# Kernel optimization log

Measured on AMD Instinct MI355X. Metric: run time of the kernel, lower is better.

Reference implementation:

```python
import jax, jax.numpy as jnp
import numpy as np

N_NODES = 100000
N_EDGES = 1000000
IN_CH, HID_CH, N_CLS = 128, 64, 40


def setup_inputs() -> dict:
    key = jax.random.key(0)
    ks = jax.random.split(key, 8)
    x = jax.random.normal(ks[0], (N_NODES, IN_CH), dtype=jnp.float32)
    edge_index = jax.random.randint(ks[1], (2, N_EDGES), 0, N_NODES, dtype=jnp.int32)
    # Glorot-ish scaled weights (ARMAConv init_weight / root_weight, K=1 stack squeezed)
    w1_init = jax.random.normal(ks[2], (IN_CH, HID_CH), dtype=jnp.float32) / np.sqrt(IN_CH)
    w1_root = jax.random.normal(ks[3], (IN_CH, HID_CH), dtype=jnp.float32) / np.sqrt(IN_CH)
    b1 = jnp.zeros((HID_CH,), dtype=jnp.float32)
    w2_init = jax.random.normal(ks[4], (HID_CH, N_CLS), dtype=jnp.float32) / np.sqrt(HID_CH)
    w2_root = jax.random.normal(ks[5], (HID_CH, N_CLS), dtype=jnp.float32) / np.sqrt(HID_CH)
    b2 = jnp.zeros((N_CLS,), dtype=jnp.float32)
    return {"x": x, "edge_index": edge_index,
            "w1_init": w1_init, "w1_root": w1_root, "b1": b1,
            "w2_init": w2_init, "w2_root": w2_root, "b2": b2}


def _arma_layer(x, row, col, norm, w_init, w_root, bias):
    # ARMAConv, num_stacks=1, num_layers=1, shared_weights=True, eval mode (dropout=id):
    # out = relu( A_hat @ (x W_init) + x W_root + b ), mean over the single stack.
    h = x @ w_init                           # [N, F_out]
    msg = norm[:, None] * h[row]             # gather from source nodes, [E, F_out]
    agg = jax.ops.segment_sum(msg, col, num_segments=N_NODES)  # scatter-add at targets
    return jax.nn.relu(agg + x @ w_root + bias)


def reference(x, edge_index, w1_init, w1_root, b1, w2_init, w2_root, b2):
    row, col = edge_index[0], edge_index[1]
    # gcn_norm, add_self_loops=False: deg over targets, norm = d^-1/2[row] * d^-1/2[col]
    deg = jax.ops.segment_sum(jnp.ones((row.shape[0],), x.dtype), col, num_segments=N_NODES)
    dinv = jnp.where(deg > 0, jax.lax.rsqrt(jnp.maximum(deg, 1e-12)), jnp.zeros_like(deg))
    norm = dinv[row] * dinv[col]
    h = _arma_layer(x, row, col, norm, w1_init, w1_root, b1)
    h = jax.nn.relu(h)  # BiARMA relu; dropout identity in eval
    return _arma_layer(h, row, col, norm, w2_init, w2_root, b2)
```

## Files before the change

kernel.cpp:

```cpp
#include <hip/hip_runtime.h>

#define N_NODES 100000
#define N_EDGES 1000000
#define IN_CH 128
#define HID_CH 64
#define N_CLS 40

#define NBUCK 782

static inline int cdiv(int a, int b) { return (a + b - 1) / b; }

__device__ __forceinline__ unsigned pack_bf2(float a, float b) {
    unsigned ua = __float_as_uint(a), ub = __float_as_uint(b);
    ua += 0x7fffu + ((ua >> 16) & 1u);
    ub += 0x7fffu + ((ub >> 16) & 1u);
    return (ua >> 16) | (ub & 0xffff0000u);
}
__device__ __forceinline__ float bf_lo(unsigned u) { return __uint_as_float(u << 16); }
__device__ __forceinline__ float bf_hi(unsigned u) { return __uint_as_float(u & 0xffff0000u); }


__global__ __launch_bounds__(256)
void bucket_count_kernel(const int* __restrict__ cols, int* __restrict__ gcount, int E) {
    __shared__ int hist[NBUCK];
    for (int i = threadIdx.x; i < NBUCK; i += 256) hist[i] = 0;
    __syncthreads();
    int per = (E + gridDim.x - 1) / gridDim.x;
    int s = blockIdx.x * per;
    int e = min(E, s + per);
    for (int j = s + threadIdx.x; j < e; j += 256)
        atomicAdd(&hist[cols[j] >> 7], 1);
    __syncthreads();
    for (int i = threadIdx.x; i < NBUCK; i += 256)
        if (hist[i]) atomicAdd(&gcount[i], hist[i]);
}


__global__ __launch_bounds__(1024)
void scan_bucket_kernel(const int* __restrict__ gcount, int* __restrict__ boff,
                        int* __restrict__ gcursor, int* __restrict__ offsets) {
    __shared__ int part[1024];
    int t = threadIdx.x;
    part[t] = (t < NBUCK) ? gcount[t] : 0;
    __syncthreads();
    for (int off = 1; off < 1024; off <<= 1) {
        int v = (t >= off) ? part[t - off] : 0;
        __syncthreads();
        part[t] += v;
        __syncthreads();
    }
    int excl = (t > 0) ? part[t - 1] : 0;
    if (t < NBUCK) { boff[t] = excl; gcursor[t] = excl; }
    if (t == NBUCK) { boff[NBUCK] = excl; offsets[N_NODES] = excl; }
}


__global__ __launch_bounds__(256)
void bucket_scatter_kernel(const int* __restrict__ rows, const int* __restrict__ cols,
                           int* __restrict__ gcursor, int* __restrict__ pedge, int E) {
    __shared__ int cur[NBUCK];
    for (int i = threadIdx.x; i < NBUCK; i += 256) cur[i] = 0;
    __syncthreads();
    int per = (E + gridDim.x - 1) / gridDim.x;
    int s = blockIdx.x * per;
    int e = min(E, s + per);
    for (int j = s + threadIdx.x; j < e; j += 256)
        atomicAdd(&cur[cols[j] >> 7], 1);
    __syncthreads();
    for (int i = threadIdx.x; i < NBUCK; i += 256) {
        int h = cur[i];
        cur[i] = h ? atomicAdd(&gcursor[i], h) : 0;
    }
    __syncthreads();
    for (int j = s + threadIdx.x; j < e; j += 256) {
        int c = cols[j];
        int pos = atomicAdd(&cur[c >> 7], 1);
        pedge[pos] = (rows[j] << 7) | (c & 127);
    }
}


__global__ __launch_bounds__(256)
void bucket_sort_kernel(const int* __restrict__ boff, const int* __restrict__ pedge,
                        int* __restrict__ srow, int* __restrict__ offsets,
                        float* __restrict__ dinv) {
    __shared__ int cnt[128];
    __shared__ int scn[128];
    __shared__ int cur[128];
    int b = blockIdx.x, t = threadIdx.x;
    if (t < 128) cnt[t] = 0;
    __syncthreads();
    int e0 = boff[b], e1 = boff[b + 1];
    for (int j = e0 + t; j < e1; j += 256)
        atomicAdd(&cnt[pedge[j] & 127], 1);
    __syncthreads();
    if (t < 128) scn[t] = cnt[t];
    __syncthreads();
    for (int off = 1; off < 128; off <<= 1) {
        int v = 0;
        if (t < 128 && t >= off) v = scn[t - off];
        __syncthreads();
        if (t < 128) scn[t] += v;
        __syncthreads();
    }
    if (t < 128) {
        int excl = (t > 0) ? scn[t - 1] : 0;
        cur[t] = excl;
        int node = b * 128 + t;
        if (node < N_NODES) {
            offsets[node] = e0 + excl;
            dinv[node] = cnt[t] ? rsqrtf((float)cnt[t]) : 0.f;
        }
    }
    __syncthreads();
    for (int j = e0 + t; j < e1; j += 256) {
        int p = pedge[j];
        int pos = atomicAdd(&cur[p & 127], 1);
        srow[e0 + pos] = p >> 7;
    }
}


template<int K, int C1, int C2>
__launch_bounds__(256, 4)
__global__ void gemm_fused_kernel(const float* __restrict__ X,
                                  const float* __restrict__ W1,
                                  const float* __restrict__ W2,
                                  const float* __restrict__ Bias,
                                  const float* __restrict__ dinv,
                                  unsigned* __restrict__ Y1b,
                                  float* __restrict__ Y2, int N) {
    constexpr int CT = C1 + C2;
    constexpr int CB = (CT - 64) / 16;
    constexpr int RPT = 4;
    constexpr int KC = 32;
    constexpr int NCHUNK = K / KC;
    static_assert(CT == 128 || CT == 80, "layout");
    static_assert(C1 % 4 == 0 && C2 % 4 == 0, "vec4");

    __shared__ float wl[KC][CT];
    __shared__ float xs[64][KC + 4];

    const int tid = threadIdx.x;
    const int r0 = blockIdx.x * 64;
    const int tcol = tid & 15;
    const int trow = tid >> 4;
    const int ca = tcol * 4;
    const int cb = 64 + tcol * CB;
    const int rbase = trow * RPT;

    float bsA[4];
#pragma unroll
    for (int j = 0; j < 4; ++j)
        bsA[j] = (ca >= C1) ? Bias[ca - C1 + j] : 0.f;
    float bsB[CB];
#pragma unroll
    for (int j = 0; j < CB; ++j)
        bsB[j] = Bias[cb - C1 + j];

    float accA[RPT][4];
    float accB[RPT][CB];
#pragma unroll
    for (int i = 0; i < RPT; ++i) {
#pragma unroll
        for (int j = 0; j < 4; ++j) accA[i][j] = 0.f;
#pragma unroll
        for (int j = 0; j < CB; ++j) accB[i][j] = 0.f;
    }

    for (int ch = 0; ch < NCHUNK; ++ch) {
        __syncthreads();
        constexpr int W1F4 = KC * C1 / 4;
        constexpr int W2F4 = KC * C2 / 4;
        for (int i = tid; i < W1F4; i += 256) {
            int kk = i / (C1 / 4);
            int f4 = i - kk * (C1 / 4);
            float4 v = *reinterpret_cast<const float4*>(&W1[(size_t)(ch * KC + kk) * C1 + f4 * 4]);
            *reinterpret_cast<float4*>(&wl[kk][f4 * 4]) = v;
        }
        for (int i = tid; i < W2F4; i += 256) {
            int kk = i / (C2 / 4);
            int f4 = i - kk * (C2 / 4);
            float4 v = *reinterpret_cast<const float4*>(&W2[(size_t)(ch * KC + kk) * C2 + f4 * 4]);
            *reinterpret_cast<float4*>(&wl[kk][C1 + f4 * 4]) = v;
        }
        constexpr int XF4 = 64 * KC / 4;
        for (int i = tid; i < XF4; i += 256) {
            int rr = i / (KC / 4);
            int k4 = i - rr * (KC / 4);
            int gr = r0 + rr;
            float4 v = make_float4(0.f, 0.f, 0.f, 0.f);
            if (gr < N)
                v = *reinterpret_cast<const float4*>(&X[(size_t)gr * K + ch * KC + k4 * 4]);
            *reinterpret_cast<float4*>(&xs[rr][k4 * 4]) = v;
        }
        __syncthreads();
#pragma unroll 8
        for (int kk = 0; kk < KC; ++kk) {
            float xv[RPT];
#pragma unroll
            for (int i = 0; i < RPT; ++i) xv[i] = xs[rbase + i][kk];
            float4 wA = *reinterpret_cast<const float4*>(&wl[kk][ca]);
            float wB[CB];
            if constexpr (CB == 4) {
                float4 w4 = *reinterpret_cast<const float4*>(&wl[kk][cb]);
                wB[0] = w4.x; wB[1] = w4.y; wB[2] = w4.z; wB[3] = w4.w;
            } else {
                wB[0] = wl[kk][cb];
            }
#pragma unroll
            for (int i = 0; i < RPT; ++i) {
                accA[i][0] = fmaf(xv[i], wA.x, accA[i][0]);
                accA[i][1] = fmaf(xv[i], wA.y, accA[i][1]);
                accA[i][2] = fmaf(xv[i], wA.z, accA[i][2]);
                accA[i][3] = fmaf(xv[i], wA.w, accA[i][3]);
#pragma unroll
                for (int j = 0; j < CB; ++j)
                    accB[i][j] = fmaf(xv[i], wB[j], accB[i][j]);
            }
        }
    }

#pragma unroll
    for (int i = 0; i < RPT; ++i) {
        int r = r0 + rbase + i;
        if (r >= N) continue;
        if (ca < C1) {
            float dr = dinv[r];
            uint2 p;
            p.x = pack_bf2(accA[i][0] * dr, accA[i][1] * dr);
            p.y = pack_bf2(accA[i][2] * dr, accA[i][3] * dr);
            *reinterpret_cast<uint2*>(&Y1b[((size_t)r * C1 + ca) >> 1]) = p;
        } else {
            float4 v = make_float4(accA[i][0] + bsA[0], accA[i][1] + bsA[1],
                                   accA[i][2] + bsA[2], accA[i][3] + bsA[3]);
            *reinterpret_cast<float4*>(&Y2[(size_t)r * C2 + (ca - C1)]) = v;
        }
        if constexpr (CB == 4) {
            float4 v = make_float4(accB[i][0] + bsB[0], accB[i][1] + bsB[1],
                                   accB[i][2] + bsB[2], accB[i][3] + bsB[3]);
            *reinterpret_cast<float4*>(&Y2[(size_t)r * C2 + (cb - C1)]) = v;
        } else {
            Y2[(size_t)r * C2 + (cb - C1)] = accB[i][0] + bsB[0];
        }
    }
}


template<int C>
__launch_bounds__(256)
__global__ void pull_bf16_kernel(const int* __restrict__ offsets,
                                 const int* __restrict__ srow,
                                 const float* __restrict__ dinv,
                                 const unsigned* __restrict__ H,
                                 float* __restrict__ Y, int N) {
    constexpr int TPE = C / 4;
    constexpr int CH = C / 2;
    int gid = blockIdx.x * blockDim.x + threadIdx.x;
    int node = gid / TPE;
    int lane = gid - node * TPE;
    if (node >= N) return;

    int e0 = offsets[node];
    int e1 = offsets[node + 1];
    float dc = dinv[node];

    float4 acc = make_float4(0.f, 0.f, 0.f, 0.f);
    int j = e0;
    for (; j + 4 <= e1; j += 4) {
        int r0 = srow[j + 0];
        int r1 = srow[j + 1];
        int r2 = srow[j + 2];
        int r3 = srow[j + 3];
        uint2 u0 = *reinterpret_cast<const uint2*>(&H[(size_t)r0 * CH + lane * 2]);
        uint2 u1 = *reinterpret_cast<const uint2*>(&H[(size_t)r1 * CH + lane * 2]);
        uint2 u2 = *reinterpret_cast<const uint2*>(&H[(size_t)r2 * CH + lane * 2]);
        uint2 u3 = *reinterpret_cast<const uint2*>(&H[(size_t)r3 * CH + lane * 2]);
        acc.x += (bf_lo(u0.x) + bf_lo(u1.x)) + (bf_lo(u2.x) + bf_lo(u3.x));
        acc.y += (bf_hi(u0.x) + bf_hi(u1.x)) + (bf_hi(u2.x) + bf_hi(u3.x));
        acc.z += (bf_lo(u0.y) + bf_lo(u1.y)) + (bf_lo(u2.y) + bf_lo(u3.y));
        acc.w += (bf_hi(u0.y) + bf_hi(u1.y)) + (bf_hi(u2.y) + bf_hi(u3.y));
    }
    for (; j < e1; ++j) {
        int r = srow[j];
        uint2 u = *reinterpret_cast<const uint2*>(&H[(size_t)r * CH + lane * 2]);
        acc.x += bf_lo(u.x);
        acc.y += bf_hi(u.x);
        acc.z += bf_lo(u.y);
        acc.w += bf_hi(u.y);
    }

    float4* Y4 = reinterpret_cast<float4*>(Y);
    size_t yi = (size_t)node * TPE + lane;
    float4 y = Y4[yi];
    y.x = fmaxf(fmaf(dc, acc.x, y.x), 0.f);
    y.y = fmaxf(fmaf(dc, acc.y, y.y), 0.f);
    y.z = fmaxf(fmaf(dc, acc.z, y.z), 0.f);
    y.w = fmaxf(fmaf(dc, acc.w, y.w), 0.f);
    Y4[yi] = y;
}


extern "C" void kernel_launch(void* const* d_in, const int* in_sizes, int n_in,
                              void* d_out, int out_size, void* d_ws, size_t ws_size,
                              hipStream_t stream) {
    const float* x       = (const float*)d_in[0];
    const int*   eidx    = (const int*)d_in[1];
    const float* w1_init = (const float*)d_in[2];
    const float* w1_root = (const float*)d_in[3];
    const float* b1      = (const float*)d_in[4];
    const float* w2_init = (const float*)d_in[5];
    const float* w2_root = (const float*)d_in[6];
    const float* b2      = (const float*)d_in[7];
    float* out = (float*)d_out;

    const int* rows = eidx;
    const int* cols = eidx + N_EDGES;

    int* wsi = (int*)d_ws;
    int*      gcount  = wsi;
    int*      boff    = wsi + 784;
    int*      gcursor = wsi + 1572;
    float*    dinv    = (float*)(wsi + 2360);
    int*      offsets = wsi + 102360;
    int*      srow    = wsi + 202364;
    unsigned* h0b     = (unsigned*)(wsi + 1202364);
    int*      pedge   = wsi + 1202364;
    float*    agg1    = (float*)(wsi + 4402364);
    unsigned* h2b     = h0b;

    hipMemsetAsync(gcount, 0, 784 * sizeof(int), stream);
    bucket_count_kernel<<<128, 256, 0, stream>>>(cols, gcount, N_EDGES);
    scan_bucket_kernel<<<1, 1024, 0, stream>>>(gcount, boff, gcursor, offsets);
    bucket_scatter_kernel<<<128, 256, 0, stream>>>(rows, cols, gcursor, pedge, N_EDGES);
    bucket_sort_kernel<<<NBUCK, 256, 0, stream>>>(boff, pedge, srow, offsets, dinv);

    const int GGRID = cdiv(N_NODES, 64);

    gemm_fused_kernel<IN_CH, HID_CH, HID_CH><<<GGRID, 256, 0, stream>>>(
        x, w1_init, w1_root, b1, dinv, h0b, agg1, N_NODES);
    pull_bf16_kernel<HID_CH><<<cdiv(N_NODES * (HID_CH / 4), 256), 256, 0, stream>>>(
        offsets, srow, dinv, h0b, agg1, N_NODES);

    gemm_fused_kernel<HID_CH, N_CLS, N_CLS><<<GGRID, 256, 0, stream>>>(
        agg1, w2_init, w2_root, b2, dinv, h2b, out, N_NODES);
    pull_bf16_kernel<N_CLS><<<cdiv(N_NODES * (N_CLS / 4), 256), 256, 0, stream>>>(
        offsets, srow, dinv, h2b, out, N_NODES);
}
```

Before: 287.5 us.

## Replace FP32 FMA dense GEMM with bf16 MFMA matrix-core kernel

The fused dual-weight GEMM now converts X and W tiles to bf16 in shared memory and computes with 16x16x32 bf16 MFMA instructions instead of scalar FP32 FMAs, with each wave handling 16 rows. The whole K dimension is staged at once, with weights transposed into a padded layout. This targets the compute cost of the two dense projections. In exchange it lowers the precision of the root/bias path (now bf16 inputs) and writes scalar, less coalesced outputs per lane.

```diff
diff --git a/kernel.cpp b/kernel.cpp
--- a/kernel.cpp
+++ b/kernel.cpp
@@ -10,11 +10,19 @@
 
 static inline int cdiv(int a, int b) { return (a + b - 1) / b; }
 
+using bf16x8 = __attribute__((ext_vector_type(8))) short;
+using f32x4  = __attribute__((ext_vector_type(4))) float;
+
 __device__ __forceinline__ unsigned pack_bf2(float a, float b) {
     unsigned ua = __float_as_uint(a), ub = __float_as_uint(b);
     ua += 0x7fffu + ((ua >> 16) & 1u);
     ub += 0x7fffu + ((ub >> 16) & 1u);
     return (ua >> 16) | (ub & 0xffff0000u);
+}
+__device__ __forceinline__ unsigned short bf16_of(float a) {
+    unsigned ua = __float_as_uint(a);
+    ua += 0x7fffu + ((ua >> 16) & 1u);
+    return (unsigned short)(ua >> 16);
 }
 __device__ __forceinline__ float bf_lo(unsigned u) { return __uint_as_float(u << 16); }
 __device__ __forceinline__ float bf_hi(unsigned u) { return __uint_as_float(u & 0xffff0000u); }
@@ -122,126 +130,102 @@
 
 
 template<int K, int C1, int C2>
-__launch_bounds__(256, 4)
-__global__ void gemm_fused_kernel(const float* __restrict__ X,
-                                  const float* __restrict__ W1,
-                                  const float* __restrict__ W2,
-                                  const float* __restrict__ Bias,
-                                  const float* __restrict__ dinv,
-                                  unsigned* __restrict__ Y1b,
-                                  float* __restrict__ Y2, int N) {
+__launch_bounds__(256)
+__global__ void gemm_mfma_fused_kernel(const float* __restrict__ X,
+                                       const float* __restrict__ W1,
+                                       const float* __restrict__ W2,
+                                       const float* __restrict__ Bias,
+                                       const float* __restrict__ dinv,
+                                       unsigned short* __restrict__ Y1b,
+                                       float* __restrict__ Y2, int N) {
     constexpr int CT = C1 + C2;
-    constexpr int CB = (CT - 64) / 16;
-    constexpr int RPT = 4;
-    constexpr int KC = 32;
-    constexpr int NCHUNK = K / KC;
-    static_assert(CT == 128 || CT == 80, "layout");
-    static_assert(C1 % 4 == 0 && C2 % 4 == 0, "vec4");
-
-    __shared__ float wl[KC][CT];
-    __shared__ float xs[64][KC + 4];
+    constexpr int NT = CT / 16;
+    constexpr int KS = K / 32;
+    constexpr int KP = (K + 8) / 2;
+    static_assert(CT % 16 == 0 && K % 32 == 0, "shape");
+    static_assert(C1 % 4 == 0 && C2 % 4 == 0, "staging vec4");
+
+    __shared__ unsigned xb[64 * KP];
+    __shared__ unsigned wt[CT * KP];
+    __shared__ float dloc[64];
 
     const int tid = threadIdx.x;
+    const int wave = tid >> 6;
+    const int lane = tid & 63;
+    const int m = lane & 15;
+    const int quad = lane >> 4;
     const int r0 = blockIdx.x * 64;
-    const int tcol = tid & 15;
-    const int trow = tid >> 4;
-    const int ca = tcol * 4;
-    const int cb = 64 + tcol * CB;
-    const int rbase = trow * RPT;
-
-    float bsA[4];
-#pragma unroll
-    for (int j = 0; j < 4; ++j)
-        bsA[j] = (ca >= C1) ? Bias[ca - C1 + j] : 0.f;
-    float bsB[CB];
-#pragma unroll
-    for (int j = 0; j < CB; ++j)
-        bsB[j] = Bias[cb - C1 + j];
-
-    float accA[RPT][4];
-    float accB[RPT][CB];
-#pragma unroll
-    for (int i = 0; i < RPT; ++i) {
-#pragma unroll
-        for (int j = 0; j < 4; ++j) accA[i][j] = 0.f;
-#pragma unroll
-        for (int j = 0; j < CB; ++j) accB[i][j] = 0.f;
-    }
-
-    for (int ch = 0; ch < NCHUNK; ++ch) {
-        __syncthreads();
-        constexpr int W1F4 = KC * C1 / 4;
-        constexpr int W2F4 = KC * C2 / 4;
-        for (int i = tid; i < W1F4; i += 256) {
-            int kk = i / (C1 / 4);
-            int f4 = i - kk * (C1 / 4);
-            float4 v = *reinterpret_cast<const float4*>(&W1[(size_t)(ch * KC + kk) * C1 + f4 * 4]);
-            *reinterpret_cast<float4*>(&wl[kk][f4 * 4]) = v;
+
+    if (tid < 64) {
+        int gr = r0 + tid;
+        dloc[tid] = (gr < N) ? dinv[gr] : 0.f;
+    }
+
+    constexpr int XIT = 64 * (K / 4);
+    for (int i = tid; i < XIT; i += 256) {
+        int rr = i / (K / 4);
+        int k4 = i - rr * (K / 4);
+        int gr = r0 + rr;
+        float4 v = make_float4(0.f, 0.f, 0.f, 0.f);
+        if (gr < N)
+            v = *reinterpret_cast<const float4*>(&X[(size_t)gr * K + k4 * 4]);
+        uint2 p;
+        p.x = pack_bf2(v.x, v.y);
+        p.y = pack_bf2(v.z, v.w);
+        *reinterpret_cast<uint2*>(&xb[rr * KP + k4 * 2]) = p;
+    }
+
+    constexpr int WIT = (K / 2) * (CT / 4);
+    for (int i = tid; i < WIT; i += 256) {
+        int kp = i / (CT / 4);
+        int c4 = i - kp * (CT / 4);
+        int k = kp * 2;
+        int c = c4 * 4;
+        float4 va, vb;
+        if (c < C1) {
+            va = *reinterpret_cast<const float4*>(&W1[(size_t)k * C1 + c]);
+            vb = *reinterpret_cast<const float4*>(&W1[(size_t)(k + 1) * C1 + c]);
+        } else {
+            va = *reinterpret_cast<const float4*>(&W2[(size_t)k * C2 + (c - C1)]);
+            vb = *reinterpret_cast<const float4*>(&W2[(size_t)(k + 1) * C2 + (c - C1)]);
         }
-        for (int i = tid; i < W2F4; i += 256) {
-            int kk = i / (C2 / 4);
-            int f4 = i - kk * (C2 / 4);
-            float4 v = *reinterpret_cast<const float4*>(&W2[(size_t)(ch * KC + kk) * C2 + f4 * 4]);
-            *reinterpret_cast<float4*>(&wl[kk][C1 + f4 * 4]) = v;
+        wt[(c + 0) * KP + kp] = pack_bf2(va.x, vb.x);
+        wt[(c + 1) * KP + kp] = pack_bf2(va.y, vb.y);
+        wt[(c + 2) * KP + kp] = pack_bf2(va.z, vb.z);
+        wt[(c + 3) * KP + kp] = pack_bf2(va.w, vb.w);
+    }
+    __syncthreads();
+
+    const int rowbase = wave * 16;
+    f32x4 acc[NT];
+#pragma unroll
+    for (int t = 0; t < NT; ++t) acc[t] = (f32x4){0.f, 0.f, 0.f, 0.f};
+
+#pragma unroll
+    for (int ks = 0; ks < KS; ++ks) {
+        bf16x8 a = *reinterpret_cast<const bf16x8*>(&xb[(rowbase + m) * KP + ks * 16 + quad * 4]);
+#pragma unroll
+        for (int t = 0; t < NT; ++t) {
+            bf16x8 b = *reinterpret_cast<const bf16x8*>(&wt[(t * 16 + m) * KP + ks * 16 + quad * 4]);
+            acc[t] = __builtin_amdgcn_mfma_f32_16x16x32_bf16(a, b, acc[t], 0, 0, 0);
         }
-        constexpr int XF4 = 64 * KC / 4;
-        for (int i = tid; i < XF4; i += 256) {
-            int rr = i / (KC / 4);
-            int k4 = i - rr * (KC / 4);
-            int gr = r0 + rr;
-            float4 v = make_float4(0.f, 0.f, 0.f, 0.f);
-            if (gr < N)
-                v = *reinterpret_cast<const float4*>(&X[(size_t)gr * K + ch * KC + k4 * 4]);
-            *reinterpret_cast<float4*>(&xs[rr][k4 * 4]) = v;
-        }
-        __syncthreads();
-#pragma unroll 8
-        for (int kk = 0; kk < KC; ++kk) {
-            float xv[RPT];
-#pragma unroll
-            for (int i = 0; i < RPT; ++i) xv[i] = xs[rbase + i][kk];
-            float4 wA = *reinterpret_cast<const float4*>(&wl[kk][ca]);
-            float wB[CB];
-            if constexpr (CB == 4) {
-                float4 w4 = *reinterpret_cast<const float4*>(&wl[kk][cb]);
-                wB[0] = w4.x; wB[1] = w4.y; wB[2] = w4.z; wB[3] = w4.w;
+    }
+
+#pragma unroll
+    for (int t = 0; t < NT; ++t) {
+        int c = t * 16 + m;
+        float bias = (c >= C1) ? Bias[c - C1] : 0.f;
+#pragma unroll
+        for (int reg = 0; reg < 4; ++reg) {
+            int rl = rowbase + quad * 4 + reg;
+            int r = r0 + rl;
+            if (r >= N) continue;
+            float v = acc[t][reg];
+            if (c < C1) {
+                Y1b[(size_t)r * C1 + c] = bf16_of(v * dloc[rl]);
             } else {
-                wB[0] = wl[kk][cb];
+                Y2[(size_t)r * C2 + (c - C1)] = v + bias;
             }
-#pragma unroll
-            for (int i = 0; i < RPT; ++i) {
-                accA[i][0] = fmaf(xv[i], wA.x, accA[i][0]);
-                accA[i][1] = fmaf(xv[i], wA.y, accA[i][1]);
-                accA[i][2] = fmaf(xv[i], wA.z, accA[i][2]);
-                accA[i][3] = fmaf(xv[i], wA.w, accA[i][3]);
-#pragma unroll
-                for (int j = 0; j < CB; ++j)
-                    accB[i][j] = fmaf(xv[i], wB[j], accB[i][j]);
-            }
-        }
-    }
-
-#pragma unroll
-    for (int i = 0; i < RPT; ++i) {
-        int r = r0 + rbase + i;
-        if (r >= N) continue;
-        if (ca < C1) {
-            float dr = dinv[r];
-            uint2 p;
-            p.x = pack_bf2(accA[i][0] * dr, accA[i][1] * dr);
-            p.y = pack_bf2(accA[i][2] * dr, accA[i][3] * dr);
-            *reinterpret_cast<uint2*>(&Y1b[((size_t)r * C1 + ca) >> 1]) = p;
-        } else {
-            float4 v = make_float4(accA[i][0] + bsA[0], accA[i][1] + bsA[1],
-                                   accA[i][2] + bsA[2], accA[i][3] + bsA[3]);
-            *reinterpret_cast<float4*>(&Y2[(size_t)r * C2 + (ca - C1)]) = v;
-        }
-        if constexpr (CB == 4) {
-            float4 v = make_float4(accB[i][0] + bsB[0], accB[i][1] + bsB[1],
-                                   accB[i][2] + bsB[2], accB[i][3] + bsB[3]);
-            *reinterpret_cast<float4*>(&Y2[(size_t)r * C2 + (cb - C1)]) = v;
-        } else {
-            Y2[(size_t)r * C2 + (cb - C1)] = accB[i][0] + bsB[0];
         }
     }
 }
@@ -337,13 +321,13 @@
 
     const int GGRID = cdiv(N_NODES, 64);
 
-    gemm_fused_kernel<IN_CH, HID_CH, HID_CH><<<GGRID, 256, 0, stream>>>(
-        x, w1_init, w1_root, b1, dinv, h0b, agg1, N_NODES);
+    gemm_mfma_fused_kernel<IN_CH, HID_CH, HID_CH><<<GGRID, 256, 0, stream>>>(
+        x, w1_init, w1_root, b1, dinv, (unsigned short*)h0b, agg1, N_NODES);
     pull_bf16_kernel<HID_CH><<<cdiv(N_NODES * (HID_CH / 4), 256), 256, 0, stream>>>(
         offsets, srow, dinv, h0b, agg1, N_NODES);
 
-    gemm_fused_kernel<HID_CH, N_CLS, N_CLS><<<GGRID, 256, 0, stream>>>(
-        agg1, w2_init, w2_root, b2, dinv, h2b, out, N_NODES);
+    gemm_mfma_fused_kernel<HID_CH, N_CLS, N_CLS><<<GGRID, 256, 0, stream>>>(
+        agg1, w2_init, w2_root, b2, dinv, (unsigned short*)h2b, out, N_NODES);
     pull_bf16_kernel<N_CLS><<<cdiv(N_NODES * (N_CLS / 4), 256), 256, 0, stream>>>(
         offsets, srow, dinv, h2b, out, N_NODES);
 }
```

New measurement: 264.5 us. -8.0%, faster.
